# Kernel optimization log

Measured on AMD Instinct MI355X. Metric: run time of the kernel, lower is better.

Reference implementation:

```python
import jax, jax.numpy as jnp
import numpy as np

TOP_K = 2
AUX_COEF = 1e-3

def setup_inputs() -> dict:
    key = jax.random.key(0)
    ks = jax.random.split(key, 5)
    B, S, H, I, E = 4, 2048, 1024, 2048, 8
    x = jax.random.normal(ks[0], (B, S, H), jnp.float32)
    gate_w = jax.random.normal(ks[1], (H, E), jnp.float32) * 0.02
    w_gate = jax.random.normal(ks[2], (E, H, I), jnp.float32) * 0.02
    w_up = jax.random.normal(ks[3], (E, H, I), jnp.float32) * 0.02
    w_down = jax.random.normal(ks[4], (E, I, H), jnp.float32) * 0.02
    return {"x": x, "gate_w": gate_w, "w_gate": w_gate, "w_up": w_up, "w_down": w_down}


def reference(x, gate_w, w_gate, w_up, w_down):
    B, S, H = x.shape
    E = gate_w.shape[1]
    xf = x.reshape(-1, H)              # [N, H]
    N = xf.shape[0]

    # Router: softmax in fp32 (matches F.softmax(..., dtype=torch.float32))
    logits = xf @ gate_w               # [N, E]
    rw = jax.nn.softmax(logits.astype(jnp.float32), axis=-1).astype(x.dtype)
    top_w, top_i = jax.lax.top_k(rw, TOP_K)            # [N, K]
    top_w = top_w / top_w.sum(axis=-1, keepdims=True)  # renormalize

    # Combine weights: comb[t, e] = sum_k top_w[t,k] * (top_i[t,k]==e)
    comb = jnp.zeros((N, E), x.dtype).at[jnp.arange(N)[:, None], top_i].add(top_w)

    # SwiGLU FFN computed densely per expert, masked/combined by router weights
    h_gate = jax.nn.silu(jnp.einsum('th,ehi->eti', xf, w_gate))   # [E, N, I]
    h_up = jnp.einsum('th,ehi->eti', xf, w_up)                    # [E, N, I]
    expert_out = jnp.einsum('eti,eih->eth', h_gate * h_up, w_down)  # [E, N, H]
    y = jnp.einsum('eth,te->th', expert_out, comb).reshape(B, S, H)

    # Load-balancing aux loss
    sel_w = jnp.take_along_axis(rw, top_i, axis=1)   # router weight of chosen experts [N, K]
    load = jnp.zeros((E,), rw.dtype).at[top_i.reshape(-1)].add(sel_w.reshape(-1))
    P_expert = load / N
    counts = jnp.zeros((E,), jnp.float32).at[top_i.reshape(-1)].add(1.0)
    P_token_expert = counts / (N * TOP_K)
    aux_loss = (P_expert * P_token_expert).sum() * E * AUX_COEF
    return y, aux_loss
```

## Files before the change

### kernel.cpp

```cpp
#include <hip/hip_runtime.h>

#define N_TOK 8192
#define H_DIM 1024
#define I_DIM 2048
#define N_EXP 8
#define TOPK  2
#define CAP   17408
#define MT_MAX 136

#define OFF_TOPK_I 0u
#define OFF_TOPK_W 65536u
#define OFF_COUNTS 131072u
#define OFF_LOAD   131104u
#define OFF_CURSOR 131136u
#define OFF_PO     131168u
#define OFF_TILE_E 131232u
#define OFF_BTOK   131840u
#define OFF_BW     201472u
#define CTRL_BYTES 271104u
#define OFF_WGT  1048576u
#define OFF_WUT  (OFF_WGT + 33554432u)
#define OFF_WDT  (OFF_WUT + 33554432u)
#define OFF_HB   (OFF_WDT + 33554432u)
#define OFF_XB   (OFF_HB + 71303168u)

typedef __attribute__((ext_vector_type(8))) short bf16x8;
typedef __attribute__((ext_vector_type(8))) unsigned short u16x8;
typedef __attribute__((ext_vector_type(4))) float f32x4;

__device__ __forceinline__ unsigned short f2bf(float f) {
  union { float f; unsigned int u; } v; v.f = f;
  unsigned int r = (v.u + 0x7FFFu + ((v.u >> 16) & 1u)) >> 16;
  return (unsigned short)r;
}
__device__ __forceinline__ u16x8 pack8(float4 a, float4 b) {
  u16x8 r;
  r[0] = f2bf(a.x); r[1] = f2bf(a.y); r[2] = f2bf(a.z); r[3] = f2bf(a.w);
  r[4] = f2bf(b.x); r[5] = f2bf(b.y); r[6] = f2bf(b.z); r[7] = f2bf(b.w);
  return r;
}
__device__ __forceinline__ f32x4 mfma32(bf16x8 a, bf16x8 b, f32x4 c) {
  return __builtin_amdgcn_mfma_f32_16x16x32_bf16(a, b, c, 0, 0, 0);
}
__device__ __forceinline__ void gll16(const void* g, void* l) {
  __builtin_amdgcn_global_load_lds(
      (const __attribute__((address_space(1))) unsigned int*)g,
      (__attribute__((address_space(3))) unsigned int*)l, 16, 0, 0);
}

__global__ __launch_bounds__(256) void k_xcast(const float* __restrict__ x,
                                               unsigned short* __restrict__ xb)
{
  int idx = blockIdx.x * 256 + threadIdx.x;
  const float4* s = (const float4*)x + (size_t)idx * 2;
  float4 a = s[0], b = s[1];
  *(u16x8*)&xb[(size_t)idx * 8] = pack8(a, b);
}

__global__ __launch_bounds__(256) void k_transpose(
    const float* __restrict__ wg, const float* __restrict__ wu, const float* __restrict__ wd,
    unsigned short* __restrict__ wgT, unsigned short* __restrict__ wuT,
    unsigned short* __restrict__ wdT)
{
  __shared__ unsigned short lds[64][65];
  int bid = blockIdx.x;
  int m = bid / 4096; int rem = bid % 4096;
  const float* src; unsigned short* dst; int R, C;
  if (m == 0)      { src = wg; dst = wgT; R = 1024; C = 2048; }
  else if (m == 1) { src = wu; dst = wuT; R = 1024; C = 2048; }
  else             { src = wd; dst = wdT; R = 2048; C = 1024; }
  int e = rem / 512; int trem = rem % 512;
  int tcc = C / 64;
  int r0 = (trem / tcc) * 64, c0 = (trem % tcc) * 64;
  size_t ebase = (size_t)e * R * C;
  dst += ebase;
  int tid = threadIdx.x;
  int lr = tid >> 3;
  int lc = (tid & 7) * 8;
#pragma unroll
  for (int p = 0; p < 2; ++p) {
    int row = p * 32 + lr;
    size_t off = ebase + (size_t)(r0 + row) * C + c0 + lc;
    float4 q0 = *(const float4*)&src[off];
    float4 q1 = *(const float4*)&src[off + 4];
    unsigned short tmp[8]; *(u16x8*)tmp = pack8(q0, q1);
#pragma unroll
    for (int j = 0; j < 8; ++j) lds[row][lc + j] = tmp[j];
  }
  __syncthreads();
#pragma unroll
  for (int p = 0; p < 2; ++p) {
    int drow = p * 32 + lr;
    unsigned short tmp[8];
#pragma unroll
    for (int j = 0; j < 8; ++j) tmp[j] = lds[lc + j][drow];
    *(u16x8*)&dst[(size_t)(c0 + drow) * R + r0 + lc] = *(const u16x8*)tmp;
  }
}

__global__ __launch_bounds__(256) void k_router(
    const float* __restrict__ x, const float* __restrict__ gw,
    int* __restrict__ topk_i, float* __restrict__ topk_w)
{
  int wave = threadIdx.x >> 6, lane = threadIdx.x & 63;
  int t = blockIdx.x * 4 + wave;
  const float* xr = x + (size_t)t * H_DIM;
  float acc[8];
#pragma unroll
  for (int e = 0; e < 8; ++e) acc[e] = 0.f;
#pragma unroll
  for (int it = 0; it < H_DIM / 64; ++it) {
    int h = it * 64 + lane;
    float xv = xr[h];
    float4 g0 = *(const float4*)&gw[h * 8];
    float4 g1 = *(const float4*)&gw[h * 8 + 4];
    acc[0] += xv * g0.x; acc[1] += xv * g0.y; acc[2] += xv * g0.z; acc[3] += xv * g0.w;
    acc[4] += xv * g1.x; acc[5] += xv * g1.y; acc[6] += xv * g1.z; acc[7] += xv * g1.w;
  }
#pragma unroll
  for (int off = 32; off > 0; off >>= 1) {
#pragma unroll
    for (int e = 0; e < 8; ++e) acc[e] += __shfl_xor(acc[e], off);
  }
  if (lane == 0) {
    float m = acc[0];
#pragma unroll
    for (int e = 1; e < 8; ++e) m = fmaxf(m, acc[e]);
    float p[8], s = 0.f;
#pragma unroll
    for (int e = 0; e < 8; ++e) { p[e] = __expf(acc[e] - m); s += p[e]; }
    float inv = 1.f / s;
#pragma unroll
    for (int e = 0; e < 8; ++e) p[e] *= inv;
    int i1 = 0;
#pragma unroll
    for (int e = 1; e < 8; ++e) if (p[e] > p[i1]) i1 = e;
    int i2 = (i1 == 0) ? 1 : 0;
#pragma unroll
    for (int e = 0; e < 8; ++e) if (e != i1 && p[e] > p[i2]) i2 = e;
    topk_i[t * 2]     = i1; topk_i[t * 2 + 1] = i2;
    topk_w[t * 2]     = p[i1]; topk_w[t * 2 + 1] = p[i2];
  }
}

__global__ __launch_bounds__(256) void k_hist(
    const int* __restrict__ topk_i, const float* __restrict__ topk_w,
    int* __restrict__ counts, float* __restrict__ loadw)
{
  __shared__ int c[8]; __shared__ float l[8];
  int tid = threadIdx.x;
  if (tid < 8) { c[tid] = 0; l[tid] = 0.f; }
  __syncthreads();
  int base = blockIdx.x * 1024 + tid * 4;
#pragma unroll
  for (int j = 0; j < 4; ++j) {
    int e = topk_i[base + j];
    float w = topk_w[base + j];
    atomicAdd(&c[e], 1);
    atomicAdd(&l[e], w);
  }
  __syncthreads();
  if (tid < 8) { atomicAdd(&counts[tid], c[tid]); atomicAdd(&loadw[tid], l[tid]); }
}

__global__ __launch_bounds__(256) void k_offsets(
    const int* __restrict__ counts, const float* __restrict__ loadw,
    int* __restrict__ po, int* __restrict__ tile_e, float* __restrict__ out)
{
  __shared__ int spo[9];
  if (threadIdx.x == 0) {
    int a = 0;
    for (int e = 0; e < 8; ++e) { spo[e] = a; po[e] = a; a += (counts[e] + 127) & ~127; }
    spo[8] = a; po[8] = a;
    float s = 0.f;
    for (int e = 0; e < 8; ++e) s += loadw[e] * (float)counts[e];
    out[(size_t)N_TOK * H_DIM] =
        s * ((float)N_EXP * 1e-3f) / ((float)N_TOK * (float)N_TOK * (float)TOPK);
  }
  __syncthreads();
  int mt = threadIdx.x;
  if (mt < MT_MAX) {
    int te = -1, beg = mt * 128;
    if (beg < spo[8]) {
      for (int e = 0; e < 8; ++e) if (beg >= spo[e] && beg < spo[e + 1]) te = e;
    }
    tile_e[mt] = te;
  }
}

__global__ __launch_bounds__(256) void k_bucket(
    const int* __restrict__ topk_i, const float* __restrict__ topk_w,
    const int* __restrict__ po, int* __restrict__ cursor,
    int* __restrict__ btok, float* __restrict__ bw)
{
  __shared__ int c[8];
  __shared__ int basee[8];
  int tid = threadIdx.x;
  if (tid < 8) c[tid] = 0;
  __syncthreads();
  int base = blockIdx.x * 1024 + tid * 4;
  int e4[4], r4[4]; float w4[4];
#pragma unroll
  for (int j = 0; j < 4; ++j) {
    int idx = base + j;
    int e = topk_i[idx];
    e4[j] = e;
    r4[j] = atomicAdd(&c[e], 1);
    int t = idx >> 1;
    float p0 = topk_w[t * 2], p1 = topk_w[t * 2 + 1];
    w4[j] = topk_w[idx] / (p0 + p1);
  }
  __syncthreads();
  if (tid < 8) basee[tid] = po[tid] + atomicAdd(&cursor[tid], c[tid]);
  __syncthreads();
#pragma unroll
  for (int j = 0; j < 4; ++j) {
    int slot = basee[e4[j]] + r4[j];
    btok[slot] = (base + j) >> 1;
    bw[slot] = w4[j];
  }
}

__global__ __launch_bounds__(256, 2) void k_gemm1(
    const unsigned short* __restrict__ xb,
    const unsigned short* __restrict__ wgT, const unsigned short* __restrict__ wuT,
    const int* __restrict__ btok, const int* __restrict__ tile_e,
    unsigned short* __restrict__ hbuf)
{
  int mt = blockIdx.x, nt = blockIdx.y;
  int e = tile_e[mt];
  if (e < 0) return;
  __shared__ unsigned short As[128 * 32];
  __shared__ unsigned short Bg[128 * 32];
  __shared__ unsigned short Bu[128 * 32];
  int tid = threadIdx.x;
  int wave = tid >> 6, lane = tid & 63;
  int wm = wave >> 1, wn = wave & 1;
  int quad = lane >> 4, l16 = lane & 15;

  int srow = lane >> 2;
  int sko  = (lane & 3) * 8;
  int ar0 = wave * 16 + srow;
  int ar1 = 64 + wave * 16 + srow;
  int t0 = btok[mt * 128 + ar0];
  int t1 = btok[mt * 128 + ar1];
  const unsigned short* ga0 = xb + (size_t)t0 * H_DIM + sko;
  const unsigned short* ga1 = xb + (size_t)t1 * H_DIM + sko;
  const unsigned short* bgb = wgT + ((size_t)e * I_DIM + nt * 128) * H_DIM;
  const unsigned short* bub = wuT + ((size_t)e * I_DIM + nt * 128) * H_DIM;
  const unsigned short* gg0 = bgb + (size_t)ar0 * H_DIM + sko;
  const unsigned short* gg1 = bgb + (size_t)ar1 * H_DIM + sko;
  const unsigned short* gu0 = bub + (size_t)ar0 * H_DIM + sko;
  const unsigned short* gu1 = bub + (size_t)ar1 * H_DIM + sko;
  unsigned lb0 = (unsigned)(wave * 16) * 32;
  unsigned lb1 = (unsigned)(64 + wave * 16) * 32;

  f32x4 accG[4][4], accU[4][4];
  f32x4 z = {0.f, 0.f, 0.f, 0.f};
#pragma unroll
  for (int i = 0; i < 4; ++i)
#pragma unroll
    for (int j = 0; j < 4; ++j) { accG[i][j] = z; accU[i][j] = z; }

  for (int k0 = 0; k0 < H_DIM; k0 += 32) {
    gll16(ga0 + k0, &As[lb0]);
    gll16(ga1 + k0, &As[lb1]);
    gll16(gg0 + k0, &Bg[lb0]);
    gll16(gg1 + k0, &Bg[lb1]);
    gll16(gu0 + k0, &Bu[lb0]);
    gll16(gu1 + k0, &Bu[lb1]);
    __syncthreads();
    bf16x8 af[4];
#pragma unroll
    for (int i = 0; i < 4; ++i)
      af[i] = *(const bf16x8*)&As[(wm * 64 + i * 16 + l16) * 32 + quad * 8];
#pragma unroll
    for (int j = 0; j < 4; ++j) {
      bf16x8 vg = *(const bf16x8*)&Bg[(wn * 64 + j * 16 + l16) * 32 + quad * 8];
      bf16x8 vu = *(const bf16x8*)&Bu[(wn * 64 + j * 16 + l16) * 32 + quad * 8];
#pragma unroll
      for (int i = 0; i < 4; ++i) {
        accG[i][j] = mfma32(af[i], vg, accG[i][j]);
        accU[i][j] = mfma32(af[i], vu, accU[i][j]);
      }
    }
    __syncthreads();
  }
#pragma unroll
  for (int i = 0; i < 4; ++i) {
#pragma unroll
    for (int r = 0; r < 4; ++r) {
      int row = mt * 128 + wm * 64 + i * 16 + quad * 4 + r;
      size_t base = (size_t)row * I_DIM + nt * 128 + wn * 64 + l16;
#pragma unroll
      for (int j = 0; j < 4; ++j) {
        float g = accG[i][j][r], u = accU[i][j][r];
        float sg = g / (1.f + __expf(-g));
        hbuf[base + j * 16] = f2bf(sg * u);
      }
    }
  }
}

__global__ __launch_bounds__(256, 2) void k_gemm2(
    const unsigned short* __restrict__ hbuf, const unsigned short* __restrict__ wdT,
    const int* __restrict__ btok, const float* __restrict__ bw,
    const int* __restrict__ tile_e, float* __restrict__ yout)
{
  int mt = blockIdx.x, nt = blockIdx.y;
  int e = tile_e[mt];
  if (e < 0) return;
  __shared__ unsigned short As[128 * 32];
  __shared__ unsigned short Bs[128 * 32];
  int tid = threadIdx.x;
  int wave = tid >> 6, lane = tid & 63;
  int wm = wave >> 1, wn = wave & 1;
  int quad = lane >> 4, l16 = lane & 15;

  int srow = lane >> 2;
  int sko  = (lane & 3) * 8;
  int ar0 = wave * 16 + srow;
  int ar1 = 64 + wave * 16 + srow;
  const unsigned short* ga0 = hbuf + (size_t)(mt * 128 + ar0) * I_DIM + sko;
  const unsigned short* ga1 = hbuf + (size_t)(mt * 128 + ar1) * I_DIM + sko;
  const unsigned short* bb = wdT + ((size_t)e * H_DIM + nt * 128) * I_DIM;
  const unsigned short* gb0 = bb + (size_t)ar0 * I_DIM + sko;
  const unsigned short* gb1 = bb + (size_t)ar1 * I_DIM + sko;
  unsigned lb0 = (unsigned)(wave * 16) * 32;
  unsigned lb1 = (unsigned)(64 + wave * 16) * 32;

  f32x4 acc[4][4];
  f32x4 z = {0.f, 0.f, 0.f, 0.f};
#pragma unroll
  for (int i = 0; i < 4; ++i)
#pragma unroll
    for (int j = 0; j < 4; ++j) acc[i][j] = z;

  for (int k0 = 0; k0 < I_DIM; k0 += 32) {
    gll16(ga0 + k0, &As[lb0]);
    gll16(ga1 + k0, &As[lb1]);
    gll16(gb0 + k0, &Bs[lb0]);
    gll16(gb1 + k0, &Bs[lb1]);
    __syncthreads();
    bf16x8 af[4];
#pragma unroll
    for (int i = 0; i < 4; ++i)
      af[i] = *(const bf16x8*)&As[(wm * 64 + i * 16 + l16) * 32 + quad * 8];
#pragma unroll
    for (int j = 0; j < 4; ++j) {
      bf16x8 vb = *(const bf16x8*)&Bs[(wn * 64 + j * 16 + l16) * 32 + quad * 8];
#pragma unroll
      for (int i = 0; i < 4; ++i) acc[i][j] = mfma32(af[i], vb, acc[i][j]);
    }
    __syncthreads();
  }
#pragma unroll
  for (int i = 0; i < 4; ++i) {
#pragma unroll
    for (int r = 0; r < 4; ++r) {
      int s = mt * 128 + wm * 64 + i * 16 + quad * 4 + r;
      int t = btok[s];
      float w = bw[s];
      int colb = nt * 128 + wn * 64 + l16;
#pragma unroll
      for (int j = 0; j < 4; ++j)
        atomicAdd(&yout[(size_t)t * H_DIM + colb + j * 16], w * acc[i][j][r]);
    }
  }
}

extern "C" void kernel_launch(void* const* d_in, const int* in_sizes, int n_in,
                              void* d_out, int out_size, void* d_ws, size_t ws_size,
                              hipStream_t stream)
{
  (void)in_sizes; (void)n_in; (void)out_size; (void)ws_size;
  const float* x  = (const float*)d_in[0];
  const float* gw = (const float*)d_in[1];
  const float* wg = (const float*)d_in[2];
  const float* wu = (const float*)d_in[3];
  const float* wd = (const float*)d_in[4];
  char* ws = (char*)d_ws;

  int*   topk_i = (int*)  (ws + OFF_TOPK_I);
  float* topk_w = (float*)(ws + OFF_TOPK_W);
  int*   counts = (int*)  (ws + OFF_COUNTS);
  float* loadw  = (float*)(ws + OFF_LOAD);
  int*   cursor = (int*)  (ws + OFF_CURSOR);
  int*   po     = (int*)  (ws + OFF_PO);
  int*   tile_e = (int*)  (ws + OFF_TILE_E);
  int*   btok   = (int*)  (ws + OFF_BTOK);
  float* bw     = (float*)(ws + OFF_BW);
  unsigned short* wgT  = (unsigned short*)(ws + OFF_WGT);
  unsigned short* wuT  = (unsigned short*)(ws + OFF_WUT);
  unsigned short* wdT  = (unsigned short*)(ws + OFF_WDT);
  unsigned short* hbuf = (unsigned short*)(ws + OFF_HB);
  unsigned short* xb   = (unsigned short*)(ws + OFF_XB);
  float* yout = (float*)d_out;

  (void)hipMemsetAsync(ws, 0, CTRL_BYTES, stream);
  (void)hipMemsetAsync(yout, 0, (size_t)N_TOK * H_DIM * sizeof(float), stream);
  k_xcast<<<(N_TOK * H_DIM) / 2048, 256, 0, stream>>>(x, xb);
  k_transpose<<<12288, 256, 0, stream>>>(wg, wu, wd, wgT, wuT, wdT);
  k_router<<<N_TOK / 4, 256, 0, stream>>>(x, gw, topk_i, topk_w);
  k_hist<<<16, 256, 0, stream>>>(topk_i, topk_w, counts, loadw);
  k_offsets<<<1, 256, 0, stream>>>(counts, loadw, po, tile_e, (float*)d_out);
  k_bucket<<<16, 256, 0, stream>>>(topk_i, topk_w, po, cursor, btok, bw);
  k_gemm1<<<dim3(MT_MAX, I_DIM / 128), 256, 0, stream>>>(xb, wgT, wuT, btok, tile_e, hbuf);
  k_gemm2<<<dim3(MT_MAX, H_DIM / 128), 256, 0, stream>>>(hbuf, wdT, btok, bw, tile_e, yout);
}
```

Baseline: 695.7 us.

## Replace atomic scatter-add in down-projection with bf16 slot buffer and gather-combine kernel

New measurement: 575.9 us. -17.2%, faster.

```diff
diff --git a/kernel.cpp b/kernel.cpp
--- a/kernel.cpp
+++ b/kernel.cpp
@@ -18,6 +18,7 @@
 #define OFF_BTOK   131840u
 #define OFF_BW     201472u
 #define CTRL_BYTES 271104u
+#define OFF_TSLOT  271104u
 #define OFF_WGT  1048576u
 #define OFF_WUT  (OFF_WGT + 33554432u)
 #define OFF_WDT  (OFF_WUT + 33554432u)
@@ -26,12 +27,17 @@
 
 typedef __attribute__((ext_vector_type(8))) short bf16x8;
 typedef __attribute__((ext_vector_type(8))) unsigned short u16x8;
+typedef __attribute__((ext_vector_type(4))) unsigned short u16x4;
 typedef __attribute__((ext_vector_type(4))) float f32x4;
 
 __device__ __forceinline__ unsigned short f2bf(float f) {
   union { float f; unsigned int u; } v; v.f = f;
   unsigned int r = (v.u + 0x7FFFu + ((v.u >> 16) & 1u)) >> 16;
   return (unsigned short)r;
+}
+__device__ __forceinline__ float bf2f(unsigned short u) {
+  union { unsigned int u; float f; } v; v.u = ((unsigned int)u) << 16;
+  return v.f;
 }
 __device__ __forceinline__ u16x8 pack8(float4 a, float4 b) {
   u16x8 r;
@@ -191,7 +197,7 @@
 __global__ __launch_bounds__(256) void k_bucket(
     const int* __restrict__ topk_i, const float* __restrict__ topk_w,
     const int* __restrict__ po, int* __restrict__ cursor,
-    int* __restrict__ btok, float* __restrict__ bw)
+    int* __restrict__ btok, float* __restrict__ bw, int* __restrict__ tslot)
 {
   __shared__ int c[8];
   __shared__ int basee[8];
@@ -215,9 +221,11 @@
   __syncthreads();
 #pragma unroll
   for (int j = 0; j < 4; ++j) {
+    int idx = base + j;
     int slot = basee[e4[j]] + r4[j];
-    btok[slot] = (base + j) >> 1;
+    btok[slot] = idx >> 1;
     bw[slot] = w4[j];
+    tslot[idx] = slot;
   }
 }
 
@@ -227,7 +235,7 @@
     const int* __restrict__ btok, const int* __restrict__ tile_e,
     unsigned short* __restrict__ hbuf)
 {
-  int mt = blockIdx.x, nt = blockIdx.y;
+  int mt = blockIdx.y, nt = blockIdx.x;
   int e = tile_e[mt];
   if (e < 0) return;
   __shared__ unsigned short As[128 * 32];
@@ -304,10 +312,9 @@
 
 __global__ __launch_bounds__(256, 2) void k_gemm2(
     const unsigned short* __restrict__ hbuf, const unsigned short* __restrict__ wdT,
-    const int* __restrict__ btok, const float* __restrict__ bw,
-    const int* __restrict__ tile_e, float* __restrict__ yout)
-{
-  int mt = blockIdx.x, nt = blockIdx.y;
+    const int* __restrict__ tile_e, unsigned short* __restrict__ obuf)
+{
+  int mt = blockIdx.y, nt = blockIdx.x;
   int e = tile_e[mt];
   if (e < 0) return;
   __shared__ unsigned short As[128 * 32];
@@ -359,14 +366,30 @@
 #pragma unroll
     for (int r = 0; r < 4; ++r) {
       int s = mt * 128 + wm * 64 + i * 16 + quad * 4 + r;
-      int t = btok[s];
-      float w = bw[s];
-      int colb = nt * 128 + wn * 64 + l16;
+      size_t base = (size_t)s * H_DIM + nt * 128 + wn * 64 + l16;
 #pragma unroll
       for (int j = 0; j < 4; ++j)
-        atomicAdd(&yout[(size_t)t * H_DIM + colb + j * 16], w * acc[i][j][r]);
+        obuf[base + j * 16] = f2bf(acc[i][j][r]);
     }
   }
+}
+
+__global__ __launch_bounds__(256) void k_final(
+    const unsigned short* __restrict__ obuf, const int* __restrict__ tslot,
+    const float* __restrict__ bw, float* __restrict__ y)
+{
+  int t = blockIdx.x;
+  int s0 = tslot[t * 2], s1 = tslot[t * 2 + 1];
+  float w0 = bw[s0], w1 = bw[s1];
+  int c = threadIdx.x * 4;
+  u16x4 o0 = *(const u16x4*)&obuf[(size_t)s0 * H_DIM + c];
+  u16x4 o1 = *(const u16x4*)&obuf[(size_t)s1 * H_DIM + c];
+  float4 r;
+  r.x = w0 * bf2f(o0[0]) + w1 * bf2f(o1[0]);
+  r.y = w0 * bf2f(o0[1]) + w1 * bf2f(o1[1]);
+  r.z = w0 * bf2f(o0[2]) + w1 * bf2f(o1[2]);
+  r.w = w0 * bf2f(o0[3]) + w1 * bf2f(o1[3]);
+  *(float4*)&y[(size_t)t * H_DIM + c] = r;
 }
 
 extern "C" void kernel_launch(void* const* d_in, const int* in_sizes, int n_in,
@@ -390,21 +413,23 @@
   int*   tile_e = (int*)  (ws + OFF_TILE_E);
   int*   btok   = (int*)  (ws + OFF_BTOK);
   float* bw     = (float*)(ws + OFF_BW);
+  int*   tslot  = (int*)  (ws + OFF_TSLOT);
   unsigned short* wgT  = (unsigned short*)(ws + OFF_WGT);
   unsigned short* wuT  = (unsigned short*)(ws + OFF_WUT);
   unsigned short* wdT  = (unsigned short*)(ws + OFF_WDT);
   unsigned short* hbuf = (unsigned short*)(ws + OFF_HB);
   unsigned short* xb   = (unsigned short*)(ws + OFF_XB);
+  unsigned short* obuf = (unsigned short*)(ws + OFF_WGT);
   float* yout = (float*)d_out;
 
   (void)hipMemsetAsync(ws, 0, CTRL_BYTES, stream);
-  (void)hipMemsetAsync(yout, 0, (size_t)N_TOK * H_DIM * sizeof(float), stream);
   k_xcast<<<(N_TOK * H_DIM) / 2048, 256, 0, stream>>>(x, xb);
   k_transpose<<<12288, 256, 0, stream>>>(wg, wu, wd, wgT, wuT, wdT);
   k_router<<<N_TOK / 4, 256, 0, stream>>>(x, gw, topk_i, topk_w);
   k_hist<<<16, 256, 0, stream>>>(topk_i, topk_w, counts, loadw);
   k_offsets<<<1, 256, 0, stream>>>(counts, loadw, po, tile_e, (float*)d_out);
-  k_bucket<<<16, 256, 0, stream>>>(topk_i, topk_w, po, cursor, btok, bw);
-  k_gemm1<<<dim3(MT_MAX, I_DIM / 128), 256, 0, stream>>>(xb, wgT, wuT, btok, tile_e, hbuf);
-  k_gemm2<<<dim3(MT_MAX, H_DIM / 128), 256, 0, stream>>>(hbuf, wdT, btok, bw, tile_e, yout);
-}
+  k_bucket<<<16, 256, 0, stream>>>(topk_i, topk_w, po, cursor, btok, bw, tslot);
+  k_gemm1<<<dim3(I_DIM / 128, MT_MAX), 256, 0, stream>>>(xb, wgT, wuT, btok, tile_e, hbuf);
+  k_gemm2<<<dim3(H_DIM / 128, MT_MAX), 256, 0, stream>>>(hbuf, wdT, tile_e, obuf);
+  k_final<<<N_TOK, 256, 0, stream>>>(obuf, tslot, bw, yout);
+}
```
